# Kernel tuning notes

Measured on AMD Instinct MI355X. Metric: run time of the kernel, lower is better.

The kernel has to match this reference:

```python
import jax, jax.numpy as jnp
import numpy as np

# --- model dims (from init_kwargs + Mamba3 args) ---
D_MODEL = 256            # hidden_dim
D_INNER = 2 * D_MODEL    # expand=2
D_STATE = 8
HEADDIM = 16
NHEADS = D_INNER // HEADDIM  # 32
CHUNK = 8
D_CONV = 4
CONV_DIM = D_INNER + 2 * D_STATE            # x,B,C share the depthwise conv
D_INPROJ = 2 * D_INNER + 2 * D_STATE + NHEADS  # z,xBC,dt
INPUT_DIM = 57
OUT_SIZE = 6
BATCH = 16
SEQLEN = 4096


def setup_inputs() -> dict:
    key = jax.random.key(0)
    ks = jax.random.split(key, 12)
    def w(k, shape, s=0.02):
        return jax.random.normal(k, shape, dtype=jnp.float32) * s
    # dt bias initialized so softplus(dt_bias) ~ [1e-3, 1e-1] (Mamba-style)
    dt0 = jnp.exp(jax.random.uniform(ks[4], (NHEADS,), minval=jnp.log(1e-3), maxval=jnp.log(1e-1)))
    dt_bias = dt0 + jnp.log(-jnp.expm1(-dt0))  # inverse softplus
    return {
        "x": jax.random.normal(ks[0], (BATCH, SEQLEN, INPUT_DIM), dtype=jnp.float32),
        "W_in": w(ks[1], (D_MODEL, INPUT_DIM)),
        "b_in": jnp.zeros((D_MODEL,), jnp.float32),
        "W_inproj": w(ks[2], (D_INPROJ, D_MODEL)),
        "conv_w": w(ks[3], (CONV_DIM, D_CONV), 0.2),
        "conv_b": jnp.zeros((CONV_DIM,), jnp.float32),
        "dt_bias": dt_bias.astype(jnp.float32),
        "A_log": jnp.log(jax.random.uniform(ks[5], (NHEADS,), minval=1.0, maxval=16.0)).astype(jnp.float32),
        "D": jnp.ones((NHEADS,), jnp.float32),
        "W_out": w(ks[6], (D_MODEL, D_INNER)),
        "W_cls": w(ks[7], (OUT_SIZE, D_MODEL)),
        "b_cls": jnp.zeros((OUT_SIZE,), jnp.float32),
    }


def reference(x, W_in, b_in, W_inproj, conv_w, conv_b, dt_bias, A_log, D, W_out, W_cls, b_cls):
    Bsz, Lq, _ = x.shape
    h = x @ W_in.T + b_in                                  # [B,L,D_MODEL]
    zxbcdt = h @ W_inproj.T                                # [B,L,D_INPROJ]
    z = zxbcdt[..., :D_INNER]
    xBC = zxbcdt[..., D_INNER:D_INNER + CONV_DIM]
    dt = zxbcdt[..., -NHEADS:]
    # causal depthwise conv1d (kernel D_CONV) + SiLU
    xp = jnp.pad(xBC, ((0, 0), (D_CONV - 1, 0), (0, 0)))
    conv = sum(xp[:, k:k + Lq, :] * conv_w[:, k] for k in range(D_CONV)) + conv_b
    xBC = jax.nn.silu(conv)
    xs = xBC[..., :D_INNER]
    Bm = xBC[..., D_INNER:D_INNER + D_STATE]               # [B,L,N]
    Cm = xBC[..., -D_STATE:]                               # [B,L,N]
    dt = jax.nn.softplus(dt + dt_bias)                     # [B,L,H]
    A = -jnp.exp(A_log)                                    # [H]
    # --- chunked SSD selective scan (SISO: scalar A per head) ---
    Nc = Lq // CHUNK
    xh = xs.reshape(Bsz, Nc, CHUNK, NHEADS, HEADDIM)
    Bc = Bm.reshape(Bsz, Nc, CHUNK, D_STATE)
    Cc = Cm.reshape(Bsz, Nc, CHUNK, D_STATE)
    dtc = dt.reshape(Bsz, Nc, CHUNK, NHEADS)
    cA = jnp.cumsum(dtc * A, axis=2)                       # [B,Nc,cs,H]
    # intra-chunk: y_i += sum_{j<=i} (C_i.B_j) exp(cA_i-cA_j) dt_j x_j
    Lmat = jnp.exp(cA[:, :, :, None, :] - cA[:, :, None, :, :])   # [B,Nc,i,j,H]
    mask = jnp.tril(jnp.ones((CHUNK, CHUNK), bool))
    Lmat = jnp.where(mask[None, None, :, :, None], Lmat, 0.0)
    CB = jnp.einsum('bcin,bcjn->bcij', Cc, Bc)
    scores = CB[..., None] * Lmat * dtc[:, :, None, :, :]
    y_intra = jnp.einsum('bcijh,bcjhp->bcihp', scores, xh)
    # per-chunk end states and decays
    dec_end = jnp.exp(cA[:, :, -1:, :] - cA)               # [B,Nc,cs,H]
    S = jnp.einsum('bcjh,bcjn,bcjhp->bchpn', dec_end * dtc, Bc, xh)
    chunk_dec = jnp.exp(cA[:, :, -1, :])                   # [B,Nc,H]
    def step(hc, inp):
        Sc, dc = inp
        return hc * dc[:, :, None, None] + Sc, hc          # emit state BEFORE chunk
    h0 = jnp.zeros((Bsz, NHEADS, HEADDIM, D_STATE), x.dtype)
    _, hprev = jax.lax.scan(step, h0, (jnp.moveaxis(S, 1, 0), jnp.moveaxis(chunk_dec, 1, 0)))
    hprev = jnp.moveaxis(hprev, 0, 1)                      # [B,Nc,H,P,N]
    y_inter = jnp.einsum('bchpn,bcin,bcih->bcihp', hprev, Cc, jnp.exp(cA))
    y = y_intra + y_inter + D[None, None, None, :, None] * xh
    y = y.reshape(Bsz, Lq, D_INNER)
    y = y * jax.nn.silu(z)                                 # z gate (no out-proj norm)
    out = y @ W_out.T                                      # [B,L,D_MODEL]
    pooled = out.mean(axis=1)                              # AdaptiveAvgPool1d(1)
    return pooled @ W_cls.T + b_cls                        # [B,OUT_SIZE]
```

## Files before the change

kernel.cpp:

```cpp
#include <hip/hip_runtime.h>
#include <math.h>

#define BATCH 16
#define SEQLEN 4096
#define INPUT_DIM 57
#define D_MODEL 256
#define D_INNER 512
#define D_STATE 8
#define HEADDIM 16
#define NHEADS 32
#define CHUNK 8
#define NC (SEQLEN/CHUNK)
#define CONV_DIM 528
#define D_INPROJ 1072
#define OUT_SIZE 6
#define NTOK (BATCH*SEQLEN)
#define SEG 32
#define NSEG (NC/SEG)

__device__ __forceinline__ unsigned short f2bf(float f) {
    unsigned v = __float_as_uint(f);
    return (unsigned short)((v + 0x7fffu + ((v >> 16) & 1u)) >> 16);
}
__device__ __forceinline__ unsigned pack_bf2(float lo, float hi) {
    unsigned r;
    asm("v_cvt_pk_bf16_f32 %0, %1, %2" : "=v"(r) : "v"(lo), "v"(hi));
    return r;
}
__device__ __forceinline__ float fsilu(float v) {
    return v * __builtin_amdgcn_rcpf(1.f + __expf(-v));
}

typedef __attribute__((ext_vector_type(8))) short bf16x8;
typedef __attribute__((ext_vector_type(4))) float f32x4;

__global__ void precompute_kernel(const float* __restrict__ W_in,
                                  const float* __restrict__ b_in,
                                  const float* __restrict__ W_inproj,
                                  const float* __restrict__ W_out,
                                  const float* __restrict__ W_cls,
                                  float* __restrict__ WcT,
                                  float* __restrict__ b_comb,
                                  unsigned short* __restrict__ Wbf,
                                  float* __restrict__ W_oc)
{
    int blk = blockIdx.x;
    int t = threadIdx.x;
    if (blk < D_INPROJ) {
        int n = blk;
        if (t < INPUT_DIM) {
            double acc = 0.0;
            for (int m = 0; m < D_MODEL; ++m)
                acc += (double)W_inproj[n*D_MODEL+m] * (double)W_in[m*INPUT_DIM+t];
            WcT[t*D_INPROJ + n] = (float)acc;
            if (n < 1024) Wbf[n*64 + t] = f2bf((float)acc);
        } else {
            if (t == INPUT_DIM) {
                double acc = 0.0;
                for (int m = 0; m < D_MODEL; ++m)
                    acc += (double)W_inproj[n*D_MODEL+m] * (double)b_in[m];
                b_comb[n] = (float)acc;
            }
            if (n < 1024 && t < 64) Wbf[n*64 + t] = 0;
        }
    } else {
        int d = blk - D_INPROJ;
        if (t < OUT_SIZE) {
            double acc = 0.0;
            for (int m = 0; m < D_MODEL; ++m)
                acc += (double)W_cls[t*D_MODEL+m] * (double)W_out[m*D_INNER+d];
            W_oc[t*D_INNER + d] = (float)acc;
        }
    }
}

#define XS(r,k)       uni[(r)*68 + (k)]
#define EX(r,c)       uni[2176 + (r)*48 + (c)]
#define ELS2(cw,h,i)  uni[3088 + (((cw)*32+(h))*8) + (i)]
#define GCO2(cw,h,j)  uni[3600 + (((cw)*32+(h))*8) + (j)]
#define SCL3(cw,h,o)  uni[(((cw)*32+(h))*48) + (o)]

__global__ __launch_bounds__(256) void fused_kernel(
    const float* __restrict__ x,
    const unsigned short* __restrict__ Wbf,
    const float* __restrict__ WcT,
    const float* __restrict__ bcomb,
    const float* __restrict__ conv_w,
    const float* __restrict__ conv_b,
    const float* __restrict__ dt_bias,
    const float* __restrict__ A_log,
    const float* __restrict__ Dvec,
    unsigned* __restrict__ SGg,
    float* __restrict__ cdec,
    float* __restrict__ partial_intra)
{
    __shared__ __attribute__((aligned(16))) float uni[4112];
    __shared__ __attribute__((aligned(16))) float Bs[2][8][12], Cs[2][8][12];
    __shared__ float dts[2][8][33], cAl[2][8][33];
    __shared__ float CBl[2][8][8];

    const int blk = blockIdx.x;
    const int b = blk >> 8, cp = blk & 255;
    const int bc0 = (b << 9) + cp*2;
    const int tid = threadIdx.x;
    const long t0 = (long)b*SEQLEN + (long)cp*16;
    const bool first = (cp == 0);

    #pragma unroll
    for (int it = 0; it < 8; ++it) {
        int idx = tid + it*256;
        int r = idx >> 6, k = idx & 63;
        float v = 0.f;
        if (k < INPUT_DIM && (r >= 16 || !first))
            v = x[(t0 - 16 + r)*INPUT_DIM + k];
        XS(r, k) = v;
    }
    __syncthreads();

    const int lane = tid & 63, wv = tid >> 6;
    const int quad = lane >> 4, mrow = lane & 15;

    bf16x8 aM[2], aH[2];
    #pragma unroll
    for (int hf = 0; hf < 2; ++hf) {
        const float* sm = &XS(16 + mrow, hf*32 + quad*8);
        const float* sh = &XS(mrow,      hf*32 + quad*8);
        unsigned* pm = (unsigned*)&aM[hf];
        unsigned* ph = (unsigned*)&aH[hf];
        #pragma unroll
        for (int j = 0; j < 4; ++j) {
            pm[j] = pack_bf2(sm[2*j], sm[2*j+1]);
            ph[j] = pack_bf2(sh[2*j], sh[2*j+1]);
        }
    }

    if (tid < 192) {
        const int col = tid % 48;
        const int grp = tid / 48;
        const int r0 = grp*5;
        const int nr = (grp == 3) ? 4 : 5;
        const float be = bcomb[1024 + col];
        float a[5];
        #pragma unroll
        for (int j = 0; j < 5; ++j) a[j] = be;
        for (int k = 0; k < INPUT_DIM; ++k) {
            const float w = WcT[(size_t)k*D_INPROJ + 1024 + col];
            #pragma unroll
            for (int j = 0; j < 5; ++j)
                if (j < nr) a[j] += w*XS(13 + r0 + j, k);
        }
        #pragma unroll
        for (int j = 0; j < 5; ++j) {
            if (j < nr) {
                int r = r0 + j;
                EX(r, col) = (first && r < 3) ? 0.f : a[j];
            }
        }
    }
    __syncthreads();

    if (tid < 32) {
        const int cw = tid >> 4, q = tid & 15;
        const int ch = 512 + q;
        const float4 cw4 = *(const float4*)&conv_w[ch*4];
        const float cb = conv_b[ch];
        float s0 = EX(cw*8+0, q), s1 = EX(cw*8+1, q), s2 = EX(cw*8+2, q);
        #pragma unroll
        for (int i = 0; i < 8; ++i) {
            float s3 = EX(cw*8+i+3, q);
            float v = cb + s0*cw4.x + s1*cw4.y + s2*cw4.z + s3*cw4.w;
            v = fsilu(v);
            if (q < 8) Bs[cw][i][q] = v; else Cs[cw][i][q-8] = v;
            s0 = s1; s1 = s2; s2 = s3;
        }
    } else if (tid >= 64 && tid < 128) {
        const int cw = (tid - 64) >> 5, h = (tid - 64) & 31;
        const float Ah = -__expf(A_log[h]);
        const float db = dt_bias[h];
        float ca = 0.f, e = 1.f;
        #pragma unroll
        for (int i = 0; i < 8; ++i) {
            float raw = EX(cw*8 + i + 3, 16 + h) + db;
            float dt = (raw > 20.f) ? raw : log1pf(__expf(raw));
            dts[cw][i][h] = dt;
            ca += dt * Ah;
            cAl[cw][i][h] = ca;
            e = __expf(ca);
            ELS2(cw, h, i) = e;
        }
        cdec[(bc0+cw)*32 + h] = e;
    }
    __syncthreads();

    if (tid < 128) {
        const int cw = tid >> 6, i = (tid >> 3) & 7, j = tid & 7;
        float s = 0.f;
        #pragma unroll
        for (int n = 0; n < 8; ++n) s += Cs[cw][i][n]*Bs[cw][j][n];
        CBl[cw][i][j] = s;
    }
    __syncthreads();

    #pragma unroll
    for (int q = 0; q < 12; ++q) {
        int idx = tid + q*256;
        int ofs = idx % 48;
        int hc  = idx / 48;
        int h2 = hc & 31, cw2 = hc >> 5;
        int i, j;
        if (ofs < 16) { i = ofs >> 2; j = ofs & 3; }
        else { int r2 = ofs - 16; i = 4 + (r2 >> 3); j = r2 & 7; }
        float v = 0.f;
        if (j <= i)
            v = CBl[cw2][i][j]
              * __expf(cAl[cw2][i][h2] - cAl[cw2][j][h2]) * dts[cw2][j][h2];
        SCL3(cw2, h2, ofs) = v;
    }
    #pragma unroll
    for (int q = 0; q < 2; ++q) {
        int idx = tid + q*256;
        int j = idx & 7; int hc = idx >> 3;
        int h2 = hc & 31, cw2 = hc >> 5;
        GCO2(cw2, h2, j) = __expf(cAl[cw2][7][h2] - cAl[cw2][j][h2]) * dts[cw2][j][h2];
    }
    __syncthreads();

    const int cw   = quad >> 1;
    const int joff = (quad & 1) * 4;
    const int srcConv = (lane + 48) & 63;
    const float zm = (quad & 1) ? 0.f : 1.f;

    #pragma unroll
    for (int t = 0; t < 8; ++t) {
        const int g   = wv + 4*t;
        const int h   = g;
        const int col = g*16 + mrow;

        const unsigned short* wpz = &Wbf[(size_t)col*64];
        bf16x8 bz0 = *(const bf16x8*)&wpz[quad*8];
        bf16x8 bz1 = *(const bf16x8*)&wpz[32 + quad*8];
        const float bvz = bcomb[col];
        f32x4 accZ; accZ.x = bvz; accZ.y = bvz; accZ.z = bvz; accZ.w = bvz;
        accZ = __builtin_amdgcn_mfma_f32_16x16x32_bf16(aM[0], bz0, accZ, 0, 0, 0);
        accZ = __builtin_amdgcn_mfma_f32_16x16x32_bf16(aM[1], bz1, accZ, 0, 0, 0);

        const unsigned short* wpx = &Wbf[(size_t)(col + 512)*64];
        bf16x8 bx0 = *(const bf16x8*)&wpx[quad*8];
        bf16x8 bx1 = *(const bf16x8*)&wpx[32 + quad*8];
        const float bvx = bcomb[col + 512];
        f32x4 accXM; accXM.x = bvx; accXM.y = bvx; accXM.z = bvx; accXM.w = bvx;
        accXM = __builtin_amdgcn_mfma_f32_16x16x32_bf16(aM[0], bx0, accXM, 0, 0, 0);
        accXM = __builtin_amdgcn_mfma_f32_16x16x32_bf16(aM[1], bx1, accXM, 0, 0, 0);
        f32x4 accXH; accXH.x = bvx; accXH.y = bvx; accXH.z = bvx; accXH.w = bvx;
        accXH = __builtin_amdgcn_mfma_f32_16x16x32_bf16(aH[0], bx0, accXH, 0, 0, 0);
        accXH = __builtin_amdgcn_mfma_f32_16x16x32_bf16(aH[1], bx1, accXH, 0, 0, 0);

        float s1 = (quad == 3) ? accXH[3] : accXM[3];
        float s2 = (quad == 3) ? accXH[2] : accXM[2];
        float s3 = (quad == 3) ? accXH[1] : accXM[1];
        float r1 = __shfl(s1, srcConv, 64);
        float r2 = __shfl(s2, srcConv, 64);
        float r3 = __shfl(s3, srcConv, 64);
        if (first && quad == 0) { r1 = 0.f; r2 = 0.f; r3 = 0.f; }

        const float4 cw4 = *(const float4*)&conv_w[col*4];
        const float cb = conv_b[col];
        float vals[7] = {r3, r2, r1, accXM[0], accXM[1], accXM[2], accXM[3]};
        float xv[4], szv[4];
        #pragma unroll
        for (int r = 0; r < 4; ++r) {
            float v = cb + vals[r]*cw4.x + vals[r+1]*cw4.y + vals[r+2]*cw4.z + vals[r+3]*cw4.w;
            xv[r] = fsilu(v);
            szv[r] = fsilu(accZ[r]);
        }

        const float* sbase = &SCL3(cw, h, 0);
        float part[8];
        #pragma unroll
        for (int i = 0; i < 4; ++i) {
            f32x4 c4 = *(const f32x4*)&sbase[i*4];
            part[i] = zm*(c4[0]*xv[0] + c4[1]*xv[1] + c4[2]*xv[2] + c4[3]*xv[3]);
        }
        #pragma unroll
        for (int i = 4; i < 8; ++i) {
            f32x4 c4 = *(const f32x4*)&sbase[16 + (i-4)*8 + joff];
            part[i] = c4[0]*xv[0] + c4[1]*xv[1] + c4[2]*xv[2] + c4[3]*xv[3];
        }

        const float Dv = Dvec[h];
        float pa = 0.f;
        #pragma unroll
        for (int r = 0; r < 4; ++r) {
            float mine   = (quad & 1) ? part[4+r] : part[r];
            float theirs = (quad & 1) ? part[r]   : part[4+r];
            float other  = __shfl_xor(theirs, 16, 64);
            float y = Dv*xv[r] + mine + other;
            pa += y * szv[r];
        }
        pa += __shfl_xor(pa, 16, 64);
        if ((quad & 1) == 0)
            partial_intra[(size_t)(bc0 + cw)*512 + col] = pa;

        f32x4 G4 = *(const f32x4*)&GCO2(cw, h, joff);
        f32x4 E4 = *(const f32x4*)&ELS2(cw, h, joff);
        float sn[8], gg[8];
        #pragma unroll
        for (int n = 0; n < 8; ++n) { sn[n] = 0.f; gg[n] = 0.f; }
        #pragma unroll
        for (int r = 0; r < 4; ++r) {
            const int il = joff + r;
            float w  = szv[r]*E4[r];
            float uu = G4[r]*xv[r];
            const float4 B0 = *(const float4*)&Bs[cw][il][0];
            const float4 B1 = *(const float4*)&Bs[cw][il][4];
            const float4 C0 = *(const float4*)&Cs[cw][il][0];
            const float4 C1 = *(const float4*)&Cs[cw][il][4];
            sn[0] += uu*B0.x; sn[1] += uu*B0.y; sn[2] += uu*B0.z; sn[3] += uu*B0.w;
            sn[4] += uu*B1.x; sn[5] += uu*B1.y; sn[6] += uu*B1.z; sn[7] += uu*B1.w;
            gg[0] += w*C0.x;  gg[1] += w*C0.y;  gg[2] += w*C0.z;  gg[3] += w*C0.w;
            gg[4] += w*C1.x;  gg[5] += w*C1.y;  gg[6] += w*C1.z;  gg[7] += w*C1.w;
        }
        unsigned up[8];
        #pragma unroll
        for (int n = 0; n < 8; ++n) {
            unsigned pk = pack_bf2(sn[n], gg[n]);
            unsigned pv = (unsigned)__shfl_xor((int)pk, 16, 64);
            float psn = __uint_as_float(pv << 16);
            float pgg = __uint_as_float(pv & 0xffff0000u);
            up[n] = pack_bf2(sn[n] + psn, gg[n] + pgg);
        }
        if ((quad & 1) == 0) {
            unsigned* dst = &SGg[((size_t)(bc0 + cw)*32 + h)*128 + mrow*8];
            *(uint4*)&dst[0] = *(uint4*)&up[0];
            *(uint4*)&dst[4] = *(uint4*)&up[4];
        }
    }
}

__global__ __launch_bounds__(128) void scanseg_kernel(
    const unsigned* __restrict__ SGg,
    const float* __restrict__ cdec,
    float* __restrict__ Sloc,
    float* __restrict__ Gseg,
    float* __restrict__ Aseg,
    float* __restrict__ ploc)
{
    const int blk = blockIdx.x;
    const int seg = blk & (NSEG-1);
    const int bh  = blk >> 4;
    const int b = bh >> 5, h = bh & 31;
    const int tid = threadIdx.x;
    const int c0 = seg*SEG;

    float s = 0.f, P = 1.f, G = 0.f, pooled = 0.f;
    const unsigned* src = &SGg[((size_t)(b*NC + c0)*32 + h)*128 + tid];
    const float* dsrc = &cdec[(b*NC + c0)*32 + h];

    #pragma unroll 4
    for (int cc = 0; cc < SEG; ++cc) {
        unsigned u = src[(size_t)cc*4096];
        float d = dsrc[cc*32];
        float Sv = __uint_as_float(u << 16);
        float gv = __uint_as_float(u & 0xffff0000u);
        pooled += s * gv;
        G += P * gv;
        P *= d;
        s = s*d + Sv;
    }
    Sloc[(size_t)blk*128 + tid] = s;
    Gseg[(size_t)blk*128 + tid] = G;
    if (tid == 0) Aseg[blk] = P;

    float t = pooled;
    t += __shfl_down(t, 4, 8);
    t += __shfl_down(t, 2, 8);
    t += __shfl_down(t, 1, 8);
    if ((tid & 7) == 0) ploc[(size_t)blk*16 + (tid >> 3)] = t;
}

__global__ __launch_bounds__(128) void scancomb_kernel(
    const float* __restrict__ Sloc,
    const float* __restrict__ Gseg,
    const float* __restrict__ Aseg,
    const float* __restrict__ ploc,
    double* __restrict__ partial_inter)
{
    __shared__ double red[128];
    const int bh = blockIdx.x;
    const int tid = threadIdx.x;
    float s = 0.f;
    double acc = 0.0;
    for (int seg = 0; seg < NSEG; ++seg) {
        size_t base = (size_t)(bh*NSEG + seg);
        float Gv = Gseg[base*128 + tid];
        float Av = Aseg[base];
        float Sv = Sloc[base*128 + tid];
        acc += (double)(s * Gv);
        s = s*Av + Sv;
    }
    red[tid] = acc;
    __syncthreads();
    if (tid < 16) {
        double t = 0.0;
        #pragma unroll
        for (int n = 0; n < 8; ++n) t += red[tid*8 + n];
        for (int seg = 0; seg < NSEG; ++seg)
            t += (double)ploc[(size_t)(bh*NSEG + seg)*16 + tid];
        partial_inter[(size_t)bh*16 + tid] = t;
    }
}

__global__ __launch_bounds__(256) void reduce_intra_kernel(
    const float* __restrict__ pIn,
    float* __restrict__ pred)
{
    const int g = blockIdx.x & 31;
    const int b = blockIdx.x >> 5;
    const int tid = threadIdx.x;
    for (int col = tid; col < 512; col += 256) {
        float s = 0.f;
        #pragma unroll 4
        for (int c = 0; c < 16; ++c)
            s += pIn[((size_t)b*NC + g*16 + c)*512 + col];
        pred[((size_t)(b*32) + g)*512 + col] = s;
    }
}

__global__ __launch_bounds__(512) void final_kernel(
    const float* __restrict__ pred,
    const double* __restrict__ partial_inter,
    const float* __restrict__ W_oc,
    const float* __restrict__ b_cls,
    float* __restrict__ out)
{
    __shared__ double pooled[512];
    const int b = blockIdx.x, tid = threadIdx.x;
    double ssum = 0.0;
    for (int g = 0; g < 32; ++g)
        ssum += (double)pred[((size_t)(b*32) + g)*512 + tid];
    ssum += partial_inter[(size_t)b*512 + tid];
    pooled[tid] = ssum * (1.0/(double)SEQLEN);
    __syncthreads();
    if (tid < OUT_SIZE*64) {
        const int o = tid >> 6, l = tid & 63;
        double acc = 0.0;
        for (int m = l; m < 512; m += 64)
            acc += pooled[m] * (double)W_oc[o*512 + m];
        #pragma unroll
        for (int off = 32; off > 0; off >>= 1)
            acc += __shfl_down(acc, off);
        if (l == 0) out[b*OUT_SIZE + o] = (float)(acc + (double)b_cls[o]);
    }
}

extern "C" void kernel_launch(void* const* d_in, const int* in_sizes, int n_in,
                              void* d_out, int out_size, void* d_ws, size_t ws_size,
                              hipStream_t stream)
{
    const float* x        = (const float*)d_in[0];
    const float* W_in     = (const float*)d_in[1];
    const float* b_in     = (const float*)d_in[2];
    const float* W_inproj = (const float*)d_in[3];
    const float* conv_w   = (const float*)d_in[4];
    const float* conv_b   = (const float*)d_in[5];
    const float* dt_bias  = (const float*)d_in[6];
    const float* A_log    = (const float*)d_in[7];
    const float* Dvec     = (const float*)d_in[8];
    const float* W_out    = (const float*)d_in[9];
    const float* W_cls    = (const float*)d_in[10];
    const float* b_cls    = (const float*)d_in[11];
    float* out = (float*)d_out;

    char* ws = (char*)d_ws;
    size_t off = 0;
    auto alloc = [&](size_t bytes) -> void* {
        void* p = ws + off;
        off += (bytes + 255) & ~(size_t)255;
        return p;
    };
    unsigned* SGg = (unsigned*)alloc((size_t)BATCH*NC*32*128*4);
    float*  cdecb = (float*) alloc((size_t)BATCH*NC*32*4);
    float*  pIn   = (float*) alloc((size_t)BATCH*NC*512*4);
    float*  SlocB = (float*) alloc((size_t)BATCH*NHEADS*NSEG*128*4);
    float*  GsegB = (float*) alloc((size_t)BATCH*NHEADS*NSEG*128*4);
    float*  AsegB = (float*) alloc((size_t)BATCH*NHEADS*NSEG*4);
    float*  plocB = (float*) alloc((size_t)BATCH*NHEADS*NSEG*16*4);
    float*  pred  = (float*) alloc((size_t)BATCH*32*512*4);
    double* pIt   = (double*)alloc((size_t)BATCH*512*8);
    float*  WcT   = (float*) alloc((size_t)INPUT_DIM*D_INPROJ*4);
    float*  bcomb = (float*) alloc((size_t)D_INPROJ*4);
    unsigned short* Wbf = (unsigned short*)alloc((size_t)1024*64*2);
    float*  Woc   = (float*) alloc((size_t)OUT_SIZE*D_INNER*4);
    if (off > ws_size) return;

    precompute_kernel<<<D_INPROJ + D_INNER, 64, 0, stream>>>(W_in, b_in, W_inproj, W_out, W_cls,
                                                             WcT, bcomb, Wbf, Woc);
    fused_kernel<<<BATCH*NC/2, 256, 0, stream>>>(x, Wbf, WcT, bcomb, conv_w, conv_b,
                                                 dt_bias, A_log, Dvec, SGg, cdecb, pIn);
    scanseg_kernel<<<BATCH*NHEADS*NSEG, 128, 0, stream>>>(SGg, cdecb, SlocB, GsegB, AsegB, plocB);
    scancomb_kernel<<<BATCH*NHEADS, 128, 0, stream>>>(SlocB, GsegB, AsegB, plocB, pIt);
    reduce_intra_kernel<<<BATCH*32, 256, 0, stream>>>(pIn, pred);
    final_kernel<<<BATCH, 512, 0, stream>>>(pred, pIt, Woc, b_cls, out);
}
```

Before: 304.5 us.

## Merge chunk pairs in-block before writing scan state to halve intermediate traffic

Each fused block now combines its two adjacent chunks' state contributions (S, G) and the cross-chunk pooled term locally via a lane shuffle before storing. That halves the SGg, cdec and partial_intra buffers and the number of steps the segment scan has to walk. The precompute dot products also get four independent double accumulators to break the serial add chain. The trade is slightly more shuffle and arithmetic in the fused kernel, plus an extra bf16 rounding step on the combined states.

```diff
diff --git a/kernel.cpp b/kernel.cpp
--- a/kernel.cpp
+++ b/kernel.cpp
@@ -11,12 +11,13 @@
 #define NHEADS 32
 #define CHUNK 8
 #define NC (SEQLEN/CHUNK)
+#define NCH (NC/2)
 #define CONV_DIM 528
 #define D_INPROJ 1072
 #define OUT_SIZE 6
 #define NTOK (BATCH*SEQLEN)
-#define SEG 32
-#define NSEG (NC/SEG)
+#define NSEG 16
+#define SEGC (NCH/NSEG)
 
 __device__ __forceinline__ unsigned short f2bf(float f) {
     unsigned v = __float_as_uint(f);
@@ -49,27 +50,40 @@
     if (blk < D_INPROJ) {
         int n = blk;
         if (t < INPUT_DIM) {
-            double acc = 0.0;
-            for (int m = 0; m < D_MODEL; ++m)
-                acc += (double)W_inproj[n*D_MODEL+m] * (double)W_in[m*INPUT_DIM+t];
+            double a0=0.0, a1=0.0, a2=0.0, a3=0.0;
+            for (int m = 0; m < D_MODEL; m += 4) {
+                a0 += (double)W_inproj[n*D_MODEL+m  ] * (double)W_in[(m  )*INPUT_DIM+t];
+                a1 += (double)W_inproj[n*D_MODEL+m+1] * (double)W_in[(m+1)*INPUT_DIM+t];
+                a2 += (double)W_inproj[n*D_MODEL+m+2] * (double)W_in[(m+2)*INPUT_DIM+t];
+                a3 += (double)W_inproj[n*D_MODEL+m+3] * (double)W_in[(m+3)*INPUT_DIM+t];
+            }
+            double acc = (a0+a1)+(a2+a3);
             WcT[t*D_INPROJ + n] = (float)acc;
             if (n < 1024) Wbf[n*64 + t] = f2bf((float)acc);
         } else {
             if (t == INPUT_DIM) {
-                double acc = 0.0;
-                for (int m = 0; m < D_MODEL; ++m)
-                    acc += (double)W_inproj[n*D_MODEL+m] * (double)b_in[m];
-                b_comb[n] = (float)acc;
+                double a0=0.0, a1=0.0, a2=0.0, a3=0.0;
+                for (int m = 0; m < D_MODEL; m += 4) {
+                    a0 += (double)W_inproj[n*D_MODEL+m  ] * (double)b_in[m  ];
+                    a1 += (double)W_inproj[n*D_MODEL+m+1] * (double)b_in[m+1];
+                    a2 += (double)W_inproj[n*D_MODEL+m+2] * (double)b_in[m+2];
+                    a3 += (double)W_inproj[n*D_MODEL+m+3] * (double)b_in[m+3];
+                }
+                b_comb[n] = (float)((a0+a1)+(a2+a3));
             }
             if (n < 1024 && t < 64) Wbf[n*64 + t] = 0;
         }
     } else {
         int d = blk - D_INPROJ;
         if (t < OUT_SIZE) {
-            double acc = 0.0;
-            for (int m = 0; m < D_MODEL; ++m)
-                acc += (double)W_cls[t*D_MODEL+m] * (double)W_out[m*D_INNER+d];
-            W_oc[t*D_INNER + d] = (float)acc;
+            double a0=0.0, a1=0.0, a2=0.0, a3=0.0;
+            for (int m = 0; m < D_MODEL; m += 4) {
+                a0 += (double)W_cls[t*D_MODEL+m  ] * (double)W_out[(m  )*D_INNER+d];
+                a1 += (double)W_cls[t*D_MODEL+m+1] * (double)W_out[(m+1)*D_INNER+d];
+                a2 += (double)W_cls[t*D_MODEL+m+2] * (double)W_out[(m+2)*D_INNER+d];
+                a3 += (double)W_cls[t*D_MODEL+m+3] * (double)W_out[(m+3)*D_INNER+d];
+            }
+            W_oc[t*D_INNER + d] = (float)((a0+a1)+(a2+a3));
         }
     }
 }
@@ -101,7 +115,7 @@
 
     const int blk = blockIdx.x;
     const int b = blk >> 8, cp = blk & 255;
-    const int bc0 = (b << 9) + cp*2;
+    const int scBase = (b << 8) + cp;
     const int tid = threadIdx.x;
     const long t0 = (long)b*SEQLEN + (long)cp*16;
     const bool first = (cp == 0);
@@ -177,7 +191,7 @@
         const int cw = (tid - 64) >> 5, h = (tid - 64) & 31;
         const float Ah = -__expf(A_log[h]);
         const float db = dt_bias[h];
-        float ca = 0.f, e = 1.f;
+        float ca = 0.f;
         #pragma unroll
         for (int i = 0; i < 8; ++i) {
             float raw = EX(cw*8 + i + 3, 16 + h) + db;
@@ -185,10 +199,8 @@
             dts[cw][i][h] = dt;
             ca += dt * Ah;
             cAl[cw][i][h] = ca;
-            e = __expf(ca);
-            ELS2(cw, h, i) = e;
-        }
-        cdec[(bc0+cw)*32 + h] = e;
+            ELS2(cw, h, i) = __expf(ca);
+        }
     }
     __syncthreads();
 
@@ -198,6 +210,9 @@
         #pragma unroll
         for (int n = 0; n < 8; ++n) s += Cs[cw][i][n]*Bs[cw][j][n];
         CBl[cw][i][j] = s;
+    } else if (tid < 160) {
+        const int h = tid - 128;
+        cdec[(size_t)scBase*32 + h] = ELS2(0, h, 7) * ELS2(1, h, 7);
     }
     __syncthreads();
 
@@ -298,8 +313,7 @@
             pa += y * szv[r];
         }
         pa += __shfl_xor(pa, 16, 64);
-        if ((quad & 1) == 0)
-            partial_intra[(size_t)(bc0 + cw)*512 + col] = pa;
+        float paO = __shfl_xor(pa, 32, 64);
 
         f32x4 G4 = *(const f32x4*)&GCO2(cw, h, joff);
         f32x4 E4 = *(const f32x4*)&ELS2(cw, h, joff);
@@ -320,17 +334,31 @@
             gg[0] += w*C0.x;  gg[1] += w*C0.y;  gg[2] += w*C0.z;  gg[3] += w*C0.w;
             gg[4] += w*C1.x;  gg[5] += w*C1.y;  gg[6] += w*C1.z;  gg[7] += w*C1.w;
         }
-        unsigned up[8];
+        float sC[8], gC[8];
         #pragma unroll
         for (int n = 0; n < 8; ++n) {
             unsigned pk = pack_bf2(sn[n], gg[n]);
             unsigned pv = (unsigned)__shfl_xor((int)pk, 16, 64);
-            float psn = __uint_as_float(pv << 16);
-            float pgg = __uint_as_float(pv & 0xffff0000u);
-            up[n] = pack_bf2(sn[n] + psn, gg[n] + pgg);
-        }
-        if ((quad & 1) == 0) {
-            unsigned* dst = &SGg[((size_t)(bc0 + cw)*32 + h)*128 + mrow*8];
+            sC[n] = sn[n] + __uint_as_float(pv << 16);
+            gC[n] = gg[n] + __uint_as_float(pv & 0xffff0000u);
+        }
+        const float d0 = ELS2(0, h, 7), d1 = ELS2(1, h, 7);
+        float local = 0.f;
+        unsigned up[8];
+        #pragma unroll
+        for (int n = 0; n < 8; ++n) {
+            unsigned pk = pack_bf2(sC[n], gC[n]);
+            unsigned pv = (unsigned)__shfl_xor((int)pk, 32, 64);
+            float So = __uint_as_float(pv << 16);
+            float go = __uint_as_float(pv & 0xffff0000u);
+            float Sp = sC[n]*d1 + So;
+            float Gp = gC[n] + d0*go;
+            local += sC[n]*go;
+            up[n] = pack_bf2(Sp, Gp);
+        }
+        if (quad == 0) {
+            partial_intra[(size_t)scBase*512 + col] = pa + paO + local;
+            unsigned* dst = &SGg[((size_t)scBase*32 + h)*128 + mrow*8];
             *(uint4*)&dst[0] = *(uint4*)&up[0];
             *(uint4*)&dst[4] = *(uint4*)&up[4];
         }
@@ -350,14 +378,14 @@
     const int bh  = blk >> 4;
     const int b = bh >> 5, h = bh & 31;
     const int tid = threadIdx.x;
-    const int c0 = seg*SEG;
+    const int c0 = seg*SEGC;
 
     float s = 0.f, P = 1.f, G = 0.f, pooled = 0.f;
-    const unsigned* src = &SGg[((size_t)(b*NC + c0)*32 + h)*128 + tid];
-    const float* dsrc = &cdec[(b*NC + c0)*32 + h];
+    const unsigned* src = &SGg[((size_t)(b*NCH + c0)*32 + h)*128 + tid];
+    const float* dsrc = &cdec[(b*NCH + c0)*32 + h];
 
     #pragma unroll 4
-    for (int cc = 0; cc < SEG; ++cc) {
+    for (int cc = 0; cc < SEGC; ++cc) {
         unsigned u = src[(size_t)cc*4096];
         float d = dsrc[cc*32];
         float Sv = __uint_as_float(u << 16);
@@ -420,8 +448,8 @@
     for (int col = tid; col < 512; col += 256) {
         float s = 0.f;
         #pragma unroll 4
-        for (int c = 0; c < 16; ++c)
-            s += pIn[((size_t)b*NC + g*16 + c)*512 + col];
+        for (int c = 0; c < 8; ++c)
+            s += pIn[((size_t)b*NCH + g*8 + c)*512 + col];
         pred[((size_t)(b*32) + g)*512 + col] = s;
     }
 }
@@ -478,9 +506,9 @@
         off += (bytes + 255) & ~(size_t)255;
         return p;
     };
-    unsigned* SGg = (unsigned*)alloc((size_t)BATCH*NC*32*128*4);
-    float*  cdecb = (float*) alloc((size_t)BATCH*NC*32*4);
-    float*  pIn   = (float*) alloc((size_t)BATCH*NC*512*4);
+    unsigned* SGg = (unsigned*)alloc((size_t)BATCH*NCH*32*128*4);
+    float*  cdecb = (float*) alloc((size_t)BATCH*NCH*32*4);
+    float*  pIn   = (float*) alloc((size_t)BATCH*NCH*512*4);
     float*  SlocB = (float*) alloc((size_t)BATCH*NHEADS*NSEG*128*4);
     float*  GsegB = (float*) alloc((size_t)BATCH*NHEADS*NSEG*128*4);
     float*  AsegB = (float*) alloc((size_t)BATCH*NHEADS*NSEG*4);
```

Measured after the change: 297.2 us. -2.4%, faster.
